# Kernel optimization log

Hardware: AMD Instinct MI355X
Metric: run time of the kernel (lower is better)

The kernel has to match this reference:

```python
import jax, jax.numpy as jnp
import numpy as np

N, E, DIM, NF, ED = 15000, 30000, 64, 3, 1

def _gru_cell(x, h, w_ih, w_hh, b_ih, b_hh):
    gi = x @ w_ih.T + b_ih
    gh = h @ w_hh.T + b_hh
    ir, iz, i_n = jnp.split(gi, 3, axis=-1)
    hr, hz, hn = jnp.split(gh, 3, axis=-1)
    r = jax.nn.sigmoid(ir + hr)
    z = jax.nn.sigmoid(iz + hz)
    n = jnp.tanh(i_n + r * hn)
    return (1.0 - z) * n + z * h

def _lstm_cell(x, h, c, w_ih, w_hh, b_ih, b_hh):
    g = x @ w_ih.T + b_ih + h @ w_hh.T + b_hh
    i, f, gg, o = jnp.split(g, 4, axis=-1)
    c2 = jax.nn.sigmoid(f) * c + jax.nn.sigmoid(i) * jnp.tanh(gg)
    return jax.nn.sigmoid(o) * jnp.tanh(c2), c2

def setup_inputs():
    key = jax.random.key(0)
    ks = jax.random.split(key, 32)
    p = lambda k, shape: jax.random.normal(k, shape, jnp.float32) * 0.05
    return {
        "x": jax.random.normal(ks[0], (N, NF), jnp.float32),
        "edge_index": jax.random.randint(ks[1], (2, E), 0, N),
        "edge_attr": jax.random.uniform(ks[2], (E, ED), jnp.float32),
        "lin0_w": p(ks[3], (DIM, NF)), "lin0_b": p(ks[4], (DIM,)),
        "e1_w": p(ks[5], (DIM, ED)), "e1_b": p(ks[6], (DIM,)),
        "e2_w": p(ks[7], (DIM * DIM, DIM)), "e2_b": p(ks[8], (DIM * DIM,)),
        "root_w": p(ks[9], (DIM, DIM)), "conv_b": p(ks[10], (DIM,)),
        "gru_w_ih": p(ks[11], (3 * DIM, DIM)), "gru_w_hh": p(ks[12], (3 * DIM, DIM)),
        "gru_b_ih": p(ks[13], (3 * DIM,)), "gru_b_hh": p(ks[14], (3 * DIM,)),
        "s2s_w_ih": p(ks[15], (4 * DIM, 2 * DIM)), "s2s_w_hh": p(ks[16], (4 * DIM, DIM)),
        "s2s_b_ih": p(ks[17], (4 * DIM,)), "s2s_b_hh": p(ks[18], (4 * DIM,)),
        "mem_w_ih": p(ks[19], (4 * DIM, 2 * DIM)), "mem_w_hh": p(ks[20], (4 * DIM, DIM)),
        "mem_b_ih": p(ks[21], (4 * DIM,)), "mem_b_hh": p(ks[22], (4 * DIM,)),
        "lin1_w": p(ks[23], (DIM, DIM)), "lin1_b": p(ks[24], (DIM,)),
        "lin3_w": p(ks[25], (1, DIM)), "lin3_b": p(ks[26], (1,)),
    }

def reference(x, edge_index, edge_attr, lin0_w, lin0_b, e1_w, e1_b, e2_w, e2_b,
              root_w, conv_b, gru_w_ih, gru_w_hh, gru_b_ih, gru_b_hh,
              s2s_w_ih, s2s_w_hh, s2s_b_ih, s2s_b_hh,
              mem_w_ih, mem_w_hh, mem_b_ih, mem_b_hh,
              lin1_w, lin1_b, lin3_w, lin3_b):
    n = x.shape[0]
    src, dst = edge_index[0], edge_index[1]
    # per-edge weight matrices from the edge MLP: [E, DIM, DIM] (edge_attr is constant across the 6 conv steps)
    he = jax.nn.relu(edge_attr @ e1_w.T + e1_b)
    We = (he @ e2_w.T + e2_b).reshape(-1, DIM, DIM)
    deg = jax.ops.segment_sum(jnp.ones(src.shape[0], jnp.float32), dst, num_segments=n)
    denom = jnp.maximum(deg, 1.0)[:, None]
    out = jax.nn.relu(x @ lin0_w.T + lin0_b)   # [N, DIM]
    h = out                                    # GRU hidden init = lin0 output
    for _ in range(6):
        msg = jnp.einsum('ei,eio->eo', out[src], We)          # gather + per-edge matmul
        agg = jax.ops.segment_sum(msg, dst, num_segments=n) / denom  # mean aggr
        m = jax.nn.relu(agg + out @ root_w + conv_b)          # NNConv root + bias
        h = _gru_cell(m, h, gru_w_ih, gru_w_hh, gru_b_ih, gru_b_hh)
        out = h
    # Set2Set pooling over a single graph (data.batch is all zeros)
    q_star = jnp.zeros((1, 2 * DIM), x.dtype)
    hs = jnp.zeros((1, DIM), x.dtype)
    cs = jnp.zeros((1, DIM), x.dtype)
    for _ in range(6):
        hs, cs = _lstm_cell(q_star, hs, cs, s2s_w_ih, s2s_w_hh, s2s_b_ih, s2s_b_hh)
        e = out @ hs[0]                     # [N] attention logits
        a = jax.nn.softmax(e)
        r = (a[:, None] * out).sum(0, keepdims=True)  # [1, DIM]
        q_star = jnp.concatenate([hs, r], axis=-1)     # [1, 2*DIM]
    hx, cx = _lstm_cell(q_star, jnp.zeros((1, DIM), x.dtype), jnp.zeros((1, DIM), x.dtype),
                        mem_w_ih, mem_w_hh, mem_b_ih, mem_b_hh)
    o = jax.nn.relu(hx @ lin1_w.T + lin1_b)
    v = o @ lin3_w.T + lin3_b               # [1, 1]
    return v, hx, cx
```

## Files before the change

### kernel.cpp

```cpp
#include <hip/hip_runtime.h>
#include <math.h>

#define Nn 15000
#define NP 15040
#define Ee 30000
#define NB_E 118
#define EB 938

#define OFF_AGG   0
#define OFF_DEG   962560
#define ZERO_END  977560
#define OFF_OUT   977568
#define OFF_DINV  1940128
#define OFF_AT    1955136
#define OFF_BT    2221376
#define OFF_BP    2487616
#define OFF_U     2487680
#define OFF_V     2491840
#define OFF_MC    2496000
#define OFF_PE    2496016
#define OFF_BH    2526016
#define OFF_BC    2533696
#define OFF_SS    2541376
#define OFF_SD    2571376
#define OFF_SA    2601376
#define OFF_SP    2631376
#define OFF_PK    2661376
#define OFF_GMA   2690048
#define OFF_GSA   2690304
#define OFF_GRA   2690560
#define OFF_GMB   2706944
#define OFF_GSB   2707200
#define OFF_GRB   2707456
#define OFF_HS    2723840
#define OFF_CS    2723904
#define OFF_TSA   2723968
#define OFF_TSB   2740352
#define OFF_TMA   2756736
#define OFF_TMB   2773120
#define WS_FLOATS 2789504

#define SB_LIN0   3760
#define SB_PAT    3760
#define SB_WT2    3761
#define SB_WT3    3873
#define SB_ZERO   4129
#define SB_TOTAL  5084
#define ZERO_F4   244390

__device__ __forceinline__ float sigf(float x) { return 1.0f / (1.0f + expf(-x)); }
__device__ __forceinline__ float bcast(float v, int l) {
    return __int_as_float(__builtin_amdgcn_readlane(__float_as_int(v), l));
}
__device__ __forceinline__ int bcasti(int v, int l) {
    return __builtin_amdgcn_readlane(v, l);
}

__global__ __launch_bounds__(256) void k_setup(
        const float* __restrict__ x, const float* __restrict__ l0w,
        const float* __restrict__ l0b, float* __restrict__ out,
        const float* __restrict__ e1w, const float* __restrict__ e1b,
        float* __restrict__ bp, float* __restrict__ u, float* __restrict__ v,
        int* __restrict__ mc,
        const float* __restrict__ rootw, const float* __restrict__ whh,
        const float* __restrict__ wih, float* __restrict__ pk,
        const float* __restrict__ swih, const float* __restrict__ swhh,
        const float* __restrict__ mwih,
        float* __restrict__ tsa, float* __restrict__ tsb,
        float* __restrict__ tma, float* __restrict__ tmb,
        float* __restrict__ zbase) {
    int b = blockIdx.x, tid = threadIdx.x;
    if (b < SB_LIN0) {
        int idx = b*256 + tid;
        int n = idx >> 6, o = idx & 63;
        float vv = 0.f;
        if (n < Nn)
            vv = fmaxf(l0b[o] + x[n*3+0]*l0w[o*3+0] + x[n*3+1]*l0w[o*3+1]
                       + x[n*3+2]*l0w[o*3+2], 0.f);
        out[idx] = vv;
    } else if (b == SB_PAT) {
        __shared__ float t[64]; __shared__ int valid[64];
        __shared__ float sbp[65]; __shared__ int cnt;
        int k = tid;
        float w1 = 0.f, b1 = 0.f, tv = 0.f; int va = 0;
        if (k < 64) {
            w1 = e1w[k]; b1 = e1b[k];
            if (w1 != 0.f) { tv = -b1 / w1; va = (tv > 0.f && tv < 1.f) ? 1 : 0; }
            t[k] = tv; valid[k] = va;
        }
        __syncthreads();
        if (k < 64 && va) {
            int rank = 0;
            for (int kk = 0; kk < 64; ++kk)
                if (valid[kk] && (t[kk] < tv || (t[kk] == tv && kk < k))) rank++;
            sbp[rank] = tv;
        }
        if (k == 0) { int c = 0; for (int kk = 0; kk < 64; ++kk) c += valid[kk]; cnt = c; *mc = c; }
        __syncthreads();
        if (k < 64) {
            int m = cnt;
            if (k < m) bp[k] = sbp[k];
            for (int j = 0; j <= m; ++j) {
                float lo = (j == 0) ? 0.f : sbp[j-1];
                float hi = (j == m) ? 1.f : sbp[j];
                float c = 0.5f * (lo + hi);
                int msk = (c * w1 + b1) > 0.f;
                u[j*64 + k] = msk ? w1 : 0.f;
                v[j*64 + k] = msk ? b1 : 0.f;
            }
        }
    } else if (b < SB_WT3) {
        int idx = (b - SB_WT2)*256 + tid;
        int g = idx >> 12;
        int t2 = idx & 4095;
        int q4 = t2 >> 2, k = t2 & 3;
        int lane = q4 & 63;
        int i4 = q4 >> 6;
        int i = i4*4 + k;
        float vv;
        if (g == 0)      vv = rootw[i*64 + lane];
        else if (g < 4)  vv = whh[((g-1)*64 + lane)*64 + i];
        else             vv = wih[((g-4)*64 + lane)*64 + i];
        pk[idx] = vv;
    } else if (b < SB_ZERO) {
        int idx = (b - SB_WT3)*256 + tid;
        int t2 = idx >> 14, r = idx & 16383;
        int i = r >> 8, g = r & 255;
        if (t2 == 0)      tsa[r] = swih[g*128 + i] + swhh[g*64 + i];
        else if (t2 == 1) tsb[r] = swih[g*128 + 64 + i];
        else if (t2 == 2) tma[r] = mwih[g*128 + i];
        else              tmb[r] = mwih[g*128 + 64 + i];
    } else {
        int idx = (b - SB_ZERO)*256 + tid;
        if (idx < ZERO_F4)
            ((float4*)zbase)[idx] = make_float4(0.f, 0.f, 0.f, 0.f);
    }
}

__global__ __launch_bounds__(256) void k_prep(
        const float* __restrict__ e2w, const float* __restrict__ e2b,
        const float* __restrict__ u, const float* __restrict__ v,
        const int* __restrict__ mc, float* __restrict__ At, float* __restrict__ Bt,
        const int* __restrict__ ei, const float* __restrict__ ea,
        const float* __restrict__ bp, float* __restrict__ deg,
        int* __restrict__ pe, int* __restrict__ bh) {
    int b = blockIdx.x, tid = threadIdx.x;
    if (b < 1040) {
        int j = b >> 4;
        if (j > *mc) return;
        int qc = b & 15;
        __shared__ float su[64], sv[64];
        if (tid < 64) { su[tid] = u[j*64+tid]; sv[tid] = v[j*64+tid]; }
        __syncthreads();
        int q = qc*256 + tid;
        int i = q >> 6, o = q & 63;
        const float* row = e2w + q*64;
        float a = 0.f, bb = 0.f;
        #pragma unroll 8
        for (int k = 0; k < 64; ++k) { float w = row[k]; a = fmaf(su[k], w, a); bb = fmaf(sv[k], w, bb); }
        At[j*4096 + o*64 + i] = a;
        Bt[j*4096 + o*64 + i] = bb + e2b[q];
    } else {
        int eb = b - 1040;
        __shared__ int lh[65];
        if (tid < 65) lh[tid] = 0;
        __syncthreads();
        int e = eb * 256 + tid;
        if (e < Ee) {
            atomicAdd(&deg[ei[Ee + e]], 1.0f);
            float a = ea[e];
            int m = *mc, p = 0;
            for (int j = 0; j < m; ++j) p += (bp[j] <= a) ? 1 : 0;
            pe[e] = p;
            atomicAdd(&lh[p], 1);
        }
        __syncthreads();
        if (tid < 65) bh[eb*65 + tid] = lh[tid];
    }
}

__global__ void k_scan2(const float* __restrict__ deg, float* __restrict__ dinv,
                        const int* __restrict__ bh, int* __restrict__ bc) {
    int tid = threadIdx.x;
    if (blockIdx.x < 59) {
        int n = blockIdx.x * 256 + tid;
        if (n < Nn) dinv[n] = 1.0f / fmaxf(deg[n], 1.0f);
        return;
    }
    __shared__ int stot[65]; __shared__ int sbase[65];
    if (tid < 65) {
        int t = 0;
        for (int b = 0; b < NB_E; ++b) t += bh[b*65 + tid];
        stot[tid] = t;
    }
    __syncthreads();
    if (tid == 0) {
        int run = 0;
        for (int j = 0; j < 65; ++j) { sbase[j] = run; run += stot[j]; }
    }
    __syncthreads();
    if (tid < 65) {
        int run = sbase[tid];
        for (int b = 0; b < NB_E; ++b) { bc[b*65 + tid] = run; run += bh[b*65 + tid]; }
    }
}

__global__ void k_scatter2(const int* __restrict__ ei, const float* __restrict__ ea,
                           const int* __restrict__ pe, const int* __restrict__ bc,
                           int* __restrict__ sS, int* __restrict__ sD,
                           float* __restrict__ sA, int* __restrict__ sP) {
    __shared__ int cur[65];
    int tid = threadIdx.x;
    if (tid < 65) cur[tid] = bc[blockIdx.x*65 + tid];
    __syncthreads();
    int e = blockIdx.x * 256 + tid;
    if (e >= Ee) return;
    int p = pe[e];
    int pos = atomicAdd(&cur[p], 1);
    sS[pos] = ei[e]; sD[pos] = ei[Ee + e]; sA[pos] = ea[e]; sP[pos] = p;
}

__global__ __launch_bounds__(256) void k_edge4(
        const int* __restrict__ sS, const int* __restrict__ sD,
        const float* __restrict__ sA, const int* __restrict__ sP,
        const float* __restrict__ out, const float* __restrict__ At,
        const float* __restrict__ Bt, const float* __restrict__ dinv,
        float* __restrict__ agg) {
    int tid = threadIdx.x, lane = tid & 63;
    int wid = (blockIdx.x * 256 + tid) >> 6;
    const int CH = 8;
    int e0 = wid * CH;
    if (e0 >= Ee) return;
    int e1 = e0 + CH; if (e1 > Ee) e1 = Ee;
    int cnt = e1 - e0;

    int eidx = e0 + lane;
    int msrc = 0, mdst = 0, mp = 0; float ma = 0.f, mdv = 0.f;
    if (lane < cnt) {
        msrc = sS[eidx]; mdst = sD[eidx]; ma = sA[eidx]; mp = sP[eidx];
        mdv = dinv[mdst];
    }

    float Ar[64], Br[64];
    int curp = -1;
    float hv_next = out[bcasti(msrc, 0)*64 + lane];
    for (int j = 0; j < cnt; ++j) {
        float hv = hv_next;
        if (j+1 < cnt) hv_next = out[bcasti(msrc, j+1)*64 + lane];
        int p = bcasti(mp, j);
        if (p != curp) {
            curp = p;
            const float4* Ap4 = (const float4*)(At + p*4096 + lane*64);
            const float4* Bp4 = (const float4*)(Bt + p*4096 + lane*64);
            #pragma unroll
            for (int q = 0; q < 16; ++q) {
                float4 av = Ap4[q], bv = Bp4[q];
                Ar[q*4+0]=av.x; Ar[q*4+1]=av.y; Ar[q*4+2]=av.z; Ar[q*4+3]=av.w;
                Br[q*4+0]=bv.x; Br[q*4+1]=bv.y; Br[q*4+2]=bv.z; Br[q*4+3]=bv.w;
            }
        }
        float a = bcast(ma, j);
        float acc0 = 0.f, acc1 = 0.f;
        #pragma unroll
        for (int i = 0; i < 64; i += 2) {
            float h0 = bcast(hv, i);
            float h1 = bcast(hv, i+1);
            acc0 = fmaf(h0, fmaf(a, Ar[i],   Br[i]),   acc0);
            acc1 = fmaf(h1, fmaf(a, Ar[i+1], Br[i+1]), acc1);
        }
        float acc = (acc0 + acc1) * bcast(mdv, j);
        atomicAdd(&agg[bcasti(mdst, j)*64 + lane], acc);
    }
}

__global__ __launch_bounds__(512, 2) void k_gru9(
        float* __restrict__ out, float* __restrict__ agg,
        const float* __restrict__ pk, const float* __restrict__ convb,
        const float* __restrict__ gbih, const float* __restrict__ gbhh) {
    __shared__ __align__(16) float wL[7*4096];
    int tid = threadIdx.x, lane = tid & 63, w = tid >> 6;
    {
        const float4* src = (const float4*)pk;
        float4* dst = (float4*)wL;
        #pragma unroll
        for (int i = 0; i < 14; ++i) dst[i*512 + tid] = src[i*512 + tid];
    }
    __syncthreads();
    const float4* wL4 = (const float4*)wL;
    int n0 = blockIdx.x*64 + w*8;

    float hv[8], mv[8], ghr[8], ghz[8], ghn[8];
    #pragma unroll
    for (int k = 0; k < 8; ++k) hv[k] = out[(n0+k)*64 + lane];

    float a0[8], a1[8], a2[8], a3[8];
    #pragma unroll
    for (int k = 0; k < 8; ++k) { a0[k]=0.f; a1[k]=0.f; a2[k]=0.f; a3[k]=0.f; }
    #pragma unroll 4
    for (int i4 = 0; i4 < 16; ++i4) {
        float4 w0 = wL4[(0*16+i4)*64 + lane];
        float4 w1 = wL4[(1*16+i4)*64 + lane];
        float4 w2 = wL4[(2*16+i4)*64 + lane];
        float4 w3 = wL4[(3*16+i4)*64 + lane];
        #pragma unroll
        for (int k = 0; k < 8; ++k) {
            float h;
            h = bcast(hv[k], i4*4+0);
            a0[k]=fmaf(h,w0.x,a0[k]); a1[k]=fmaf(h,w1.x,a1[k]);
            a2[k]=fmaf(h,w2.x,a2[k]); a3[k]=fmaf(h,w3.x,a3[k]);
            h = bcast(hv[k], i4*4+1);
            a0[k]=fmaf(h,w0.y,a0[k]); a1[k]=fmaf(h,w1.y,a1[k]);
            a2[k]=fmaf(h,w2.y,a2[k]); a3[k]=fmaf(h,w3.y,a3[k]);
            h = bcast(hv[k], i4*4+2);
            a0[k]=fmaf(h,w0.z,a0[k]); a1[k]=fmaf(h,w1.z,a1[k]);
            a2[k]=fmaf(h,w2.z,a2[k]); a3[k]=fmaf(h,w3.z,a3[k]);
            h = bcast(hv[k], i4*4+3);
            a0[k]=fmaf(h,w0.w,a0[k]); a1[k]=fmaf(h,w1.w,a1[k]);
            a2[k]=fmaf(h,w2.w,a2[k]); a3[k]=fmaf(h,w3.w,a3[k]);
        }
    }
    float cbv = convb[lane];
    #pragma unroll
    for (int k = 0; k < 8; ++k) {
        int gi = (n0+k)*64 + lane;
        float av = agg[gi]; agg[gi] = 0.f;
        mv[k] = fmaxf(a0[k] + av + cbv, 0.f);
        ghr[k] = a1[k]; ghz[k] = a2[k]; ghn[k] = a3[k];
    }

    #pragma unroll
    for (int k = 0; k < 8; ++k) { a0[k]=0.f; a1[k]=0.f; a2[k]=0.f; }
    #pragma unroll 4
    for (int i4 = 0; i4 < 16; ++i4) {
        float4 w4v = wL4[(4*16+i4)*64 + lane];
        float4 w5v = wL4[(5*16+i4)*64 + lane];
        float4 w6v = wL4[(6*16+i4)*64 + lane];
        #pragma unroll
        for (int k = 0; k < 8; ++k) {
            float h;
            h = bcast(mv[k], i4*4+0);
            a0[k]=fmaf(h,w4v.x,a0[k]); a1[k]=fmaf(h,w5v.x,a1[k]); a2[k]=fmaf(h,w6v.x,a2[k]);
            h = bcast(mv[k], i4*4+1);
            a0[k]=fmaf(h,w4v.y,a0[k]); a1[k]=fmaf(h,w5v.y,a1[k]); a2[k]=fmaf(h,w6v.y,a2[k]);
            h = bcast(mv[k], i4*4+2);
            a0[k]=fmaf(h,w4v.z,a0[k]); a1[k]=fmaf(h,w5v.z,a1[k]); a2[k]=fmaf(h,w6v.z,a2[k]);
            h = bcast(mv[k], i4*4+3);
            a0[k]=fmaf(h,w4v.w,a0[k]); a1[k]=fmaf(h,w5v.w,a1[k]); a2[k]=fmaf(h,w6v.w,a2[k]);
        }
    }

    float br  = gbih[lane]      + gbhh[lane];
    float bz  = gbih[64+lane]   + gbhh[64+lane];
    float bnI = gbih[128+lane];
    float bnH = gbhh[128+lane];
    #pragma unroll
    for (int k = 0; k < 8; ++k) {
        float r  = sigf(a0[k] + ghr[k] + br);
        float z  = sigf(a1[k] + ghz[k] + bz);
        float nn = tanhf(fmaf(r, ghn[k] + bnH, a2[k] + bnI));
        out[(n0+k)*64 + lane] = (1.f - z)*nn + z*hv[k];
    }
}

__global__ __launch_bounds__(512) void k_s2s(
        const float* __restrict__ tsa, const float* __restrict__ tsb,
        const float* __restrict__ bih, const float* __restrict__ bhh,
        float* __restrict__ hs, float* __restrict__ cs,
        const float* __restrict__ out,
        const float* __restrict__ gmax_rd, const float* __restrict__ gsum_rd,
        const float* __restrict__ gr_rd,
        float* __restrict__ gmax_wr, float* __restrict__ gsum_wr,
        float* __restrict__ gr_wr, int it) {
    __shared__ float red[512], shs[64], scs[64], srv[64], sg[256];
    __shared__ float wred[8], zred[8];
    __shared__ float sm_m[8], sm_z[8], sm_r[8][64];
    int tid = threadIdx.x, lane = tid & 63, w = tid >> 6;
    if (it == 0) {
        if (tid < 64) { shs[tid] = 0.f; scs[tid] = 0.f; srv[tid] = 0.f; }
        __syncthreads();
    } else {
        float gm = (tid < 256) ? gmax_rd[tid] : -3.4e38f;
        float wm = gm;
        #pragma unroll
        for (int off = 32; off > 0; off >>= 1) wm = fmaxf(wm, __shfl_xor(wm, off, 64));
        if (lane == 0) wred[w] = wm;
        __syncthreads();
        float M = fmaxf(fmaxf(fmaxf(wred[0], wred[1]), fmaxf(wred[2], wred[3])),
                        fmaxf(fmaxf(wred[4], wred[5]), fmaxf(wred[6], wred[7])));
        float zt = (tid < 256) ? gsum_rd[tid] * expf(gm - M) : 0.f;
        #pragma unroll
        for (int off = 32; off > 0; off >>= 1) zt += __shfl_xor(zt, off, 64);
        if (lane == 0) zred[w] = zt;
        float racc = 0.f;
        for (int b2 = w; b2 < 256; b2 += 8)
            racc = fmaf(gr_rd[b2*64 + lane], expf(gmax_rd[b2] - M), racc);
        red[tid] = racc;
        if (tid < 64) { shs[tid] = hs[tid]; scs[tid] = cs[tid]; }
        __syncthreads();
        if (w == 0) {
            float Z = zred[0]+zred[1]+zred[2]+zred[3]+zred[4]+zred[5]+zred[6]+zred[7];
            float s = 0.f;
            #pragma unroll
            for (int k = 0; k < 8; ++k) s += red[k*64 + lane];
            srv[lane] = s / Z;
        }
        __syncthreads();
    }
    if (tid < 256) {
        float g = bih[tid] + bhh[tid];
        #pragma unroll 8
        for (int i = 0; i < 64; ++i)
            g += shs[i]*tsa[i*256 + tid] + srv[i]*tsb[i*256 + tid];
        sg[tid] = g;
    }
    __syncthreads();
    if (tid < 64) {
        float ii = sigf(sg[tid]), ff = sigf(sg[64+tid]);
        float gg = tanhf(sg[128+tid]), oo = sigf(sg[192+tid]);
        float c2 = ff*scs[tid] + ii*gg;
        float hn = oo*tanhf(c2);
        shs[tid] = hn;
        if (blockIdx.x == 0) { hs[tid] = hn; cs[tid] = c2; }
    }
    __syncthreads();
    float hsv = shs[lane];
    float m = -3.4e38f, Z2 = 0.f, racc2 = 0.f;
    for (int n = blockIdx.x*8 + w; n < Nn; n += 2048) {
        float ov = out[n*64 + lane];
        float p = ov * hsv;
        #pragma unroll
        for (int off = 32; off > 0; off >>= 1) p += __shfl_xor(p, off, 64);
        float mn = fmaxf(m, p);
        float sc = expf(m - mn);
        float t  = expf(p - mn);
        Z2 = fmaf(Z2, sc, t);
        racc2 = fmaf(racc2, sc, t*ov);
        m = mn;
    }
    if (lane == 0) { sm_m[w] = m; sm_z[w] = Z2; }
    sm_r[w][lane] = racc2;
    __syncthreads();
    if (w == 0) {
        float M = sm_m[0];
        #pragma unroll
        for (int j = 1; j < 8; ++j) M = fmaxf(M, sm_m[j]);
        float Zb = 0.f, rb = 0.f;
        #pragma unroll
        for (int j = 0; j < 8; ++j) {
            float e = expf(sm_m[j] - M);
            Zb = fmaf(sm_z[j], e, Zb);
            rb = fmaf(sm_r[j][lane], e, rb);
        }
        gr_wr[blockIdx.x*64 + lane] = rb;
        if (lane == 0) { gmax_wr[blockIdx.x] = M; gsum_wr[blockIdx.x] = Zb; }
    }
}

__global__ __launch_bounds__(256) void k_final2(
        const float* __restrict__ tma, const float* __restrict__ tmb,
        const float* __restrict__ mbih, const float* __restrict__ mbhh,
        const float* __restrict__ hs,
        const float* __restrict__ gmax, const float* __restrict__ gsum,
        const float* __restrict__ gr,
        const float* __restrict__ l1w, const float* __restrict__ l1b,
        const float* __restrict__ l3w, const float* __restrict__ l3b,
        float* __restrict__ dout) {
    __shared__ float red[256], shs[64], srv[64], sg[256], shx[64], so[64];
    __shared__ float wred[4], zred[4];
    int tid = threadIdx.x, lane = tid & 63, w = tid >> 6;
    {
        float gm = gmax[tid];
        float wm = gm;
        #pragma unroll
        for (int off = 32; off > 0; off >>= 1) wm = fmaxf(wm, __shfl_xor(wm, off, 64));
        if (lane == 0) wred[w] = wm;
        __syncthreads();
        float M = fmaxf(fmaxf(wred[0], wred[1]), fmaxf(wred[2], wred[3]));
        float zt = gsum[tid] * expf(gm - M);
        #pragma unroll
        for (int off = 32; off > 0; off >>= 1) zt += __shfl_xor(zt, off, 64);
        if (lane == 0) zred[w] = zt;
        float racc = 0.f;
        for (int b2 = w; b2 < 256; b2 += 4)
            racc = fmaf(gr[b2*64 + lane], expf(gmax[b2] - M), racc);
        red[tid] = racc;
        if (tid < 64) shs[tid] = hs[tid];
        __syncthreads();
        if (w == 0) {
            float Z = zred[0]+zred[1]+zred[2]+zred[3];
            srv[lane] = (red[lane] + red[64+lane] + red[128+lane] + red[192+lane]) / Z;
        }
    }
    __syncthreads();
    {
        float g = mbih[tid] + mbhh[tid];
        #pragma unroll 8
        for (int i = 0; i < 64; ++i)
            g += shs[i]*tma[i*256 + tid] + srv[i]*tmb[i*256 + tid];
        sg[tid] = g;
    }
    __syncthreads();
    if (tid < 64) {
        float ii = sigf(sg[tid]);
        float gg = tanhf(sg[128+tid]);
        float oo = sigf(sg[192+tid]);
        float c2 = ii * gg;
        float hx = oo * tanhf(c2);
        shx[tid] = hx;
        dout[1 + tid] = hx;
        dout[65 + tid] = c2;
    }
    __syncthreads();
    if (tid < 64) {
        float a = l1b[tid];
        const float* wr = l1w + tid*64;
        #pragma unroll 8
        for (int i = 0; i < 64; ++i) a = fmaf(shx[i], wr[i], a);
        so[tid] = fmaxf(a, 0.f);
    }
    __syncthreads();
    if (tid == 0) {
        float v = l3b[0];
        for (int i = 0; i < 64; ++i) v = fmaf(so[i], l3w[i], v);
        dout[0] = v;
    }
}

extern "C" void kernel_launch(void* const* d_in, const int* in_sizes, int n_in,
                              void* d_out, int out_size, void* d_ws, size_t ws_size,
                              hipStream_t stream) {
    const float* x    = (const float*)d_in[0];
    const int*   ei   = (const int*)  d_in[1];
    const float* ea   = (const float*)d_in[2];
    const float* l0w  = (const float*)d_in[3];
    const float* l0b  = (const float*)d_in[4];
    const float* e1w  = (const float*)d_in[5];
    const float* e1b  = (const float*)d_in[6];
    const float* e2w  = (const float*)d_in[7];
    const float* e2b  = (const float*)d_in[8];
    const float* rootw= (const float*)d_in[9];
    const float* convb= (const float*)d_in[10];
    const float* gwih = (const float*)d_in[11];
    const float* gwhh = (const float*)d_in[12];
    const float* gbih = (const float*)d_in[13];
    const float* gbhh = (const float*)d_in[14];
    const float* swih = (const float*)d_in[15];
    const float* swhh = (const float*)d_in[16];
    const float* sbih = (const float*)d_in[17];
    const float* sbhh = (const float*)d_in[18];
    const float* mwih = (const float*)d_in[19];
    const float* mbih = (const float*)d_in[21];
    const float* mbhh = (const float*)d_in[22];
    const float* l1w  = (const float*)d_in[23];
    const float* l1b  = (const float*)d_in[24];
    const float* l3w  = (const float*)d_in[25];
    const float* l3b  = (const float*)d_in[26];

    float* ws   = (float*)d_ws;
    float* dout = (float*)d_out;
    if (ws_size < (size_t)WS_FLOATS * sizeof(float)) return;

    float* agg  = ws + OFF_AGG;
    float* deg  = ws + OFF_DEG;
    float* out  = ws + OFF_OUT;
    float* dinv = ws + OFF_DINV;
    float* At   = ws + OFF_AT;
    float* Bt   = ws + OFF_BT;
    float* bp   = ws + OFF_BP;
    float* ubuf = ws + OFF_U;
    float* vbuf = ws + OFF_V;
    int*   mc   = (int*)(ws + OFF_MC);
    int*   pe   = (int*)(ws + OFF_PE);
    int*   bh   = (int*)(ws + OFF_BH);
    int*   bc   = (int*)(ws + OFF_BC);
    int*   sS   = (int*)(ws + OFF_SS);
    int*   sD   = (int*)(ws + OFF_SD);
    float* sA   = ws + OFF_SA;
    int*   sP   = (int*)(ws + OFF_SP);
    float* pk   = ws + OFF_PK;
    float* gmA  = ws + OFF_GMA;
    float* gsA  = ws + OFF_GSA;
    float* grA  = ws + OFF_GRA;
    float* gmB  = ws + OFF_GMB;
    float* gsB  = ws + OFF_GSB;
    float* grB  = ws + OFF_GRB;
    float* hs   = ws + OFF_HS;
    float* cs   = ws + OFF_CS;
    float* tsa  = ws + OFF_TSA;
    float* tsb  = ws + OFF_TSB;
    float* tma  = ws + OFF_TMA;
    float* tmb  = ws + OFF_TMB;

    k_setup   <<<SB_TOTAL, 256, 0, stream>>>(x, l0w, l0b, out, e1w, e1b, bp, ubuf,
                                             vbuf, mc, rootw, gwhh, gwih, pk,
                                             swih, swhh, mwih, tsa, tsb, tma, tmb,
                                             ws + OFF_AGG);
    k_prep    <<<1040 + NB_E, 256, 0, stream>>>(e2w, e2b, ubuf, vbuf, mc, At, Bt,
                                                ei, ea, bp, deg, pe, bh);
    k_scan2   <<<60, 256, 0, stream>>>(deg, dinv, bh, bc);
    k_scatter2<<<NB_E, 256, 0, stream>>>(ei, ea, pe, bc, sS, sD, sA, sP);

    for (int s = 0; s < 6; ++s) {
        k_edge4<<<EB, 256, 0, stream>>>(sS, sD, sA, sP, out, At, Bt, dinv, agg);
        k_gru9 <<<NP/64, 512, 0, stream>>>(out, agg, pk, convb, gbih, gbhh);
    }

    for (int it = 0; it < 6; ++it) {
        float* gm_rd = (it & 1) ? gmA : gmB;
        float* gs_rd = (it & 1) ? gsA : gsB;
        float* gr_rd = (it & 1) ? grA : grB;
        float* gm_wr = (it & 1) ? gmB : gmA;
        float* gs_wr = (it & 1) ? gsB : gsA;
        float* gr_wr = (it & 1) ? grB : grA;
        k_s2s<<<256, 512, 0, stream>>>(tsa, tsb, sbih, sbhh, hs, cs, out,
                                       gm_rd, gs_rd, gr_rd, gm_wr, gs_wr, gr_wr, it);
    }

    k_final2<<<1, 256, 0, stream>>>(tma, tmb, mbih, mbhh, hs, gmB, gsB, grB,
                                    l1w, l1b, l3w, l3b, dout);
}
```

Baseline: 436.2 us.

## Fuse setup, prep, scan and scatter kernels; prefetch GRU inputs; double-buffer s2s state

The four setup launches (setup, prep, scan, scatter) become two. Every block that needs the edge-weight breakpoints now recomputes them in shared memory instead of reading them from a separate pass. The scatter kernel computes its own per-block prefix offsets from the histogram, so the separate scan pass goes away. The GRU kernel issues its loads of the node state and aggregation before staging the weights into shared memory, to overlap that latency, and the Set2Set hidden and cell state are ping-ponged between two buffers. The trade-offs are redundant per-block breakpoint and prefix work, and a dependence on the zeroing blocks running before the degree atomics in the same grid.

After: 439.3 us. No clear change (+0.7%).

```diff
diff --git a/kernel.cpp b/kernel.cpp
--- a/kernel.cpp
+++ b/kernel.cpp
@@ -14,13 +14,8 @@
 #define OFF_DINV  1940128
 #define OFF_AT    1955136
 #define OFF_BT    2221376
-#define OFF_BP    2487616
-#define OFF_U     2487680
-#define OFF_V     2491840
-#define OFF_MC    2496000
 #define OFF_PE    2496016
 #define OFF_BH    2526016
-#define OFF_BC    2533696
 #define OFF_SS    2541376
 #define OFF_SD    2571376
 #define OFF_SA    2601376
@@ -32,21 +27,23 @@
 #define OFF_GMB   2706944
 #define OFF_GSB   2707200
 #define OFF_GRB   2707456
-#define OFF_HS    2723840
-#define OFF_CS    2723904
 #define OFF_TSA   2723968
 #define OFF_TSB   2740352
 #define OFF_TMA   2756736
 #define OFF_TMB   2773120
-#define WS_FLOATS 2789504
-
-#define SB_LIN0   3760
-#define SB_PAT    3760
-#define SB_WT2    3761
-#define SB_WT3    3873
-#define SB_ZERO   4129
-#define SB_TOTAL  5084
-#define ZERO_F4   244390
+#define OFF_HSA   2789504
+#define OFF_CSA   2789568
+#define OFF_HSB   2789632
+#define OFF_CSB   2789696
+#define WS_FLOATS 2789760
+
+#define SA_L0_END   3760
+#define SA_WT2_END  3872
+#define SA_WT3_END  4128
+#define SA_Z_END    5083
+#define SA_AB_END   6123
+#define SA_EP_END   6241
+#define ZERO_F4     244390
 
 __device__ __forceinline__ float sigf(float x) { return 1.0f / (1.0f + expf(-x)); }
 __device__ __forceinline__ float bcast(float v, int l) {
@@ -56,21 +53,23 @@
     return __builtin_amdgcn_readlane(v, l);
 }
 
-__global__ __launch_bounds__(256) void k_setup(
+__global__ __launch_bounds__(256) void k_setupAll(
         const float* __restrict__ x, const float* __restrict__ l0w,
         const float* __restrict__ l0b, float* __restrict__ out,
         const float* __restrict__ e1w, const float* __restrict__ e1b,
-        float* __restrict__ bp, float* __restrict__ u, float* __restrict__ v,
-        int* __restrict__ mc,
+        const float* __restrict__ e2w, const float* __restrict__ e2b,
+        float* __restrict__ At, float* __restrict__ Bt,
         const float* __restrict__ rootw, const float* __restrict__ whh,
         const float* __restrict__ wih, float* __restrict__ pk,
         const float* __restrict__ swih, const float* __restrict__ swhh,
         const float* __restrict__ mwih,
         float* __restrict__ tsa, float* __restrict__ tsb,
         float* __restrict__ tma, float* __restrict__ tmb,
-        float* __restrict__ zbase) {
+        float* __restrict__ zbase,
+        const int* __restrict__ ei, const float* __restrict__ ea,
+        float* __restrict__ deg, int* __restrict__ pe, int* __restrict__ bh) {
     int b = blockIdx.x, tid = threadIdx.x;
-    if (b < SB_LIN0) {
+    if (b < SA_L0_END) {
         int idx = b*256 + tid;
         int n = idx >> 6, o = idx & 63;
         float vv = 0.f;
@@ -78,39 +77,8 @@
             vv = fmaxf(l0b[o] + x[n*3+0]*l0w[o*3+0] + x[n*3+1]*l0w[o*3+1]
                        + x[n*3+2]*l0w[o*3+2], 0.f);
         out[idx] = vv;
-    } else if (b == SB_PAT) {
-        __shared__ float t[64]; __shared__ int valid[64];
-        __shared__ float sbp[65]; __shared__ int cnt;
-        int k = tid;
-        float w1 = 0.f, b1 = 0.f, tv = 0.f; int va = 0;
-        if (k < 64) {
-            w1 = e1w[k]; b1 = e1b[k];
-            if (w1 != 0.f) { tv = -b1 / w1; va = (tv > 0.f && tv < 1.f) ? 1 : 0; }
-            t[k] = tv; valid[k] = va;
-        }
-        __syncthreads();
-        if (k < 64 && va) {
-            int rank = 0;
-            for (int kk = 0; kk < 64; ++kk)
-                if (valid[kk] && (t[kk] < tv || (t[kk] == tv && kk < k))) rank++;
-            sbp[rank] = tv;
-        }
-        if (k == 0) { int c = 0; for (int kk = 0; kk < 64; ++kk) c += valid[kk]; cnt = c; *mc = c; }
-        __syncthreads();
-        if (k < 64) {
-            int m = cnt;
-            if (k < m) bp[k] = sbp[k];
-            for (int j = 0; j <= m; ++j) {
-                float lo = (j == 0) ? 0.f : sbp[j-1];
-                float hi = (j == m) ? 1.f : sbp[j];
-                float c = 0.5f * (lo + hi);
-                int msk = (c * w1 + b1) > 0.f;
-                u[j*64 + k] = msk ? w1 : 0.f;
-                v[j*64 + k] = msk ? b1 : 0.f;
-            }
-        }
-    } else if (b < SB_WT3) {
-        int idx = (b - SB_WT2)*256 + tid;
+    } else if (b < SA_WT2_END) {
+        int idx = (b - SA_L0_END)*256 + tid;
         int g = idx >> 12;
         int t2 = idx & 4095;
         int q4 = t2 >> 2, k = t2 & 3;
@@ -122,35 +90,49 @@
         else if (g < 4)  vv = whh[((g-1)*64 + lane)*64 + i];
         else             vv = wih[((g-4)*64 + lane)*64 + i];
         pk[idx] = vv;
-    } else if (b < SB_ZERO) {
-        int idx = (b - SB_WT3)*256 + tid;
+    } else if (b < SA_WT3_END) {
+        int idx = (b - SA_WT2_END)*256 + tid;
         int t2 = idx >> 14, r = idx & 16383;
         int i = r >> 8, g = r & 255;
         if (t2 == 0)      tsa[r] = swih[g*128 + i] + swhh[g*64 + i];
         else if (t2 == 1) tsb[r] = swih[g*128 + 64 + i];
         else if (t2 == 2) tma[r] = mwih[g*128 + i];
         else              tmb[r] = mwih[g*128 + 64 + i];
-    } else {
-        int idx = (b - SB_ZERO)*256 + tid;
+    } else if (b < SA_Z_END) {
+        int idx = (b - SA_WT3_END)*256 + tid;
         if (idx < ZERO_F4)
             ((float4*)zbase)[idx] = make_float4(0.f, 0.f, 0.f, 0.f);
-    }
-}
-
-__global__ __launch_bounds__(256) void k_prep(
-        const float* __restrict__ e2w, const float* __restrict__ e2b,
-        const float* __restrict__ u, const float* __restrict__ v,
-        const int* __restrict__ mc, float* __restrict__ At, float* __restrict__ Bt,
-        const int* __restrict__ ei, const float* __restrict__ ea,
-        const float* __restrict__ bp, float* __restrict__ deg,
-        int* __restrict__ pe, int* __restrict__ bh) {
-    int b = blockIdx.x, tid = threadIdx.x;
-    if (b < 1040) {
-        int j = b >> 4;
-        if (j > *mc) return;
-        int qc = b & 15;
+    } else if (b < SA_AB_END) {
+        __shared__ float t[64]; __shared__ int valid[64];
+        __shared__ float sbp[65]; __shared__ int cnt;
         __shared__ float su[64], sv[64];
-        if (tid < 64) { su[tid] = u[j*64+tid]; sv[tid] = v[j*64+tid]; }
+        int rel = b - SA_Z_END;
+        int j = rel >> 4, qc = rel & 15;
+        float w1 = 0.f, b1 = 0.f, tv = 0.f; int va = 0;
+        if (tid < 64) {
+            w1 = e1w[tid]; b1 = e1b[tid];
+            if (w1 != 0.f) { tv = -b1 / w1; va = (tv > 0.f && tv < 1.f) ? 1 : 0; }
+            t[tid] = tv; valid[tid] = va;
+        }
+        __syncthreads();
+        if (tid < 64 && va) {
+            int rank = 0;
+            for (int kk = 0; kk < 64; ++kk)
+                if (valid[kk] && (t[kk] < tv || (t[kk] == tv && kk < tid))) rank++;
+            sbp[rank] = tv;
+        }
+        if (tid == 0) { int c = 0; for (int kk = 0; kk < 64; ++kk) c += valid[kk]; cnt = c; }
+        __syncthreads();
+        int m = cnt;
+        if (j > m) return;
+        if (tid < 64) {
+            float lo = (j == 0) ? 0.f : sbp[j-1];
+            float hi = (j == m) ? 1.f : sbp[j];
+            float c = 0.5f * (lo + hi);
+            int msk = (c * w1 + b1) > 0.f;
+            su[tid] = msk ? w1 : 0.f;
+            sv[tid] = msk ? b1 : 0.f;
+        }
         __syncthreads();
         int q = qc*256 + tid;
         int i = q >> 6, o = q & 63;
@@ -161,16 +143,33 @@
         At[j*4096 + o*64 + i] = a;
         Bt[j*4096 + o*64 + i] = bb + e2b[q];
     } else {
-        int eb = b - 1040;
+        __shared__ float t[64]; __shared__ int valid[64];
+        __shared__ float sbp[65]; __shared__ int cnt;
         __shared__ int lh[65];
+        int eb = b - SA_AB_END;
+        float w1 = 0.f, b1 = 0.f, tv = 0.f; int va = 0;
+        if (tid < 64) {
+            w1 = e1w[tid]; b1 = e1b[tid];
+            if (w1 != 0.f) { tv = -b1 / w1; va = (tv > 0.f && tv < 1.f) ? 1 : 0; }
+            t[tid] = tv; valid[tid] = va;
+        }
         if (tid < 65) lh[tid] = 0;
         __syncthreads();
+        if (tid < 64 && va) {
+            int rank = 0;
+            for (int kk = 0; kk < 64; ++kk)
+                if (valid[kk] && (t[kk] < tv || (t[kk] == tv && kk < tid))) rank++;
+            sbp[rank] = tv;
+        }
+        if (tid == 0) { int c = 0; for (int kk = 0; kk < 64; ++kk) c += valid[kk]; cnt = c; }
+        __syncthreads();
+        int m = cnt;
         int e = eb * 256 + tid;
         if (e < Ee) {
             atomicAdd(&deg[ei[Ee + e]], 1.0f);
             float a = ea[e];
-            int m = *mc, p = 0;
-            for (int j = 0; j < m; ++j) p += (bp[j] <= a) ? 1 : 0;
+            int p = 0;
+            for (int jj = 0; jj < m; ++jj) p += (sbp[jj] <= a) ? 1 : 0;
             pe[e] = p;
             atomicAdd(&lh[p], 1);
         }
@@ -179,19 +178,28 @@
     }
 }
 
-__global__ void k_scan2(const float* __restrict__ deg, float* __restrict__ dinv,
-                        const int* __restrict__ bh, int* __restrict__ bc) {
+__global__ __launch_bounds__(256) void k_scatter3(
+        const float* __restrict__ deg, float* __restrict__ dinv,
+        const int* __restrict__ ei, const float* __restrict__ ea,
+        const int* __restrict__ pe, const int* __restrict__ bh,
+        int* __restrict__ sS, int* __restrict__ sD,
+        float* __restrict__ sA, int* __restrict__ sP) {
     int tid = threadIdx.x;
     if (blockIdx.x < 59) {
         int n = blockIdx.x * 256 + tid;
         if (n < Nn) dinv[n] = 1.0f / fmaxf(deg[n], 1.0f);
         return;
     }
-    __shared__ int stot[65]; __shared__ int sbase[65];
+    int eb = blockIdx.x - 59;
+    __shared__ int stot[65], sown[65], sbase[65], cur[65];
     if (tid < 65) {
-        int t = 0;
-        for (int b = 0; b < NB_E; ++b) t += bh[b*65 + tid];
-        stot[tid] = t;
+        int own = 0, tot = 0;
+        for (int b2 = 0; b2 < NB_E; ++b2) {
+            int v = bh[b2*65 + tid];
+            if (b2 < eb) own += v;
+            tot += v;
+        }
+        stot[tid] = tot; sown[tid] = own;
     }
     __syncthreads();
     if (tid == 0) {
@@ -199,21 +207,9 @@
         for (int j = 0; j < 65; ++j) { sbase[j] = run; run += stot[j]; }
     }
     __syncthreads();
-    if (tid < 65) {
-        int run = sbase[tid];
-        for (int b = 0; b < NB_E; ++b) { bc[b*65 + tid] = run; run += bh[b*65 + tid]; }
-    }
-}
-
-__global__ void k_scatter2(const int* __restrict__ ei, const float* __restrict__ ea,
-                           const int* __restrict__ pe, const int* __restrict__ bc,
-                           int* __restrict__ sS, int* __restrict__ sD,
-                           float* __restrict__ sA, int* __restrict__ sP) {
-    __shared__ int cur[65];
-    int tid = threadIdx.x;
-    if (tid < 65) cur[tid] = bc[blockIdx.x*65 + tid];
-    __syncthreads();
-    int e = blockIdx.x * 256 + tid;
+    if (tid < 65) cur[tid] = sbase[tid] + sown[tid];
+    __syncthreads();
+    int e = eb * 256 + tid;
     if (e >= Ee) return;
     int p = pe[e];
     int pos = atomicAdd(&cur[p], 1);
@@ -279,6 +275,18 @@
         const float* __restrict__ gbih, const float* __restrict__ gbhh) {
     __shared__ __align__(16) float wL[7*4096];
     int tid = threadIdx.x, lane = tid & 63, w = tid >> 6;
+    int n0 = blockIdx.x*64 + w*8;
+
+    float hv[8], av[8];
+    #pragma unroll
+    for (int k = 0; k < 8; ++k) hv[k] = out[(n0+k)*64 + lane];
+    #pragma unroll
+    for (int k = 0; k < 8; ++k) {
+        int gi = (n0+k)*64 + lane;
+        av[k] = agg[gi];
+        agg[gi] = 0.f;
+    }
+
     {
         const float4* src = (const float4*)pk;
         float4* dst = (float4*)wL;
@@ -287,12 +295,8 @@
     }
     __syncthreads();
     const float4* wL4 = (const float4*)wL;
-    int n0 = blockIdx.x*64 + w*8;
-
-    float hv[8], mv[8], ghr[8], ghz[8], ghn[8];
-    #pragma unroll
-    for (int k = 0; k < 8; ++k) hv[k] = out[(n0+k)*64 + lane];
-
+
+    float mv[8], ghr[8], ghz[8], ghn[8];
     float a0[8], a1[8], a2[8], a3[8];
     #pragma unroll
     for (int k = 0; k < 8; ++k) { a0[k]=0.f; a1[k]=0.f; a2[k]=0.f; a3[k]=0.f; }
@@ -322,9 +326,7 @@
     float cbv = convb[lane];
     #pragma unroll
     for (int k = 0; k < 8; ++k) {
-        int gi = (n0+k)*64 + lane;
-        float av = agg[gi]; agg[gi] = 0.f;
-        mv[k] = fmaxf(a0[k] + av + cbv, 0.f);
+        mv[k] = fmaxf(a0[k] + av[k] + cbv, 0.f);
         ghr[k] = a1[k]; ghz[k] = a2[k]; ghn[k] = a3[k];
     }
 
@@ -365,7 +367,8 @@
 __global__ __launch_bounds__(512) void k_s2s(
         const float* __restrict__ tsa, const float* __restrict__ tsb,
         const float* __restrict__ bih, const float* __restrict__ bhh,
-        float* __restrict__ hs, float* __restrict__ cs,
+        const float* __restrict__ hs_rd, const float* __restrict__ cs_rd,
+        float* __restrict__ hs_wr, float* __restrict__ cs_wr,
         const float* __restrict__ out,
         const float* __restrict__ gmax_rd, const float* __restrict__ gsum_rd,
         const float* __restrict__ gr_rd,
@@ -395,7 +398,7 @@
         for (int b2 = w; b2 < 256; b2 += 8)
             racc = fmaf(gr_rd[b2*64 + lane], expf(gmax_rd[b2] - M), racc);
         red[tid] = racc;
-        if (tid < 64) { shs[tid] = hs[tid]; scs[tid] = cs[tid]; }
+        if (tid < 64) { shs[tid] = hs_rd[tid]; scs[tid] = cs_rd[tid]; }
         __syncthreads();
         if (w == 0) {
             float Z = zred[0]+zred[1]+zred[2]+zred[3]+zred[4]+zred[5]+zred[6]+zred[7];
@@ -420,7 +423,7 @@
         float c2 = ff*scs[tid] + ii*gg;
         float hn = oo*tanhf(c2);
         shs[tid] = hn;
-        if (blockIdx.x == 0) { hs[tid] = hn; cs[tid] = c2; }
+        if (blockIdx.x == 0) { hs_wr[tid] = hn; cs_wr[tid] = c2; }
     }
     __syncthreads();
     float hsv = shs[lane];
@@ -566,13 +569,8 @@
     float* dinv = ws + OFF_DINV;
     float* At   = ws + OFF_AT;
     float* Bt   = ws + OFF_BT;
-    float* bp   = ws + OFF_BP;
-    float* ubuf = ws + OFF_U;
-    float* vbuf = ws + OFF_V;
-    int*   mc   = (int*)(ws + OFF_MC);
     int*   pe   = (int*)(ws + OFF_PE);
     int*   bh   = (int*)(ws + OFF_BH);
-    int*   bc   = (int*)(ws + OFF_BC);
     int*   sS   = (int*)(ws + OFF_SS);
     int*   sD   = (int*)(ws + OFF_SD);
     float* sA   = ws + OFF_SA;
@@ -584,21 +582,21 @@
     float* gmB  = ws + OFF_GMB;
     float* gsB  = ws + OFF_GSB;
     float* grB  = ws + OFF_GRB;
-    float* hs   = ws + OFF_HS;
-    float* cs   = ws + OFF_CS;
     float* tsa  = ws + OFF_TSA;
     float* tsb  = ws + OFF_TSB;
     float* tma  = ws + OFF_TMA;
     float* tmb  = ws + OFF_TMB;
-
-    k_setup   <<<SB_TOTAL, 256, 0, stream>>>(x, l0w, l0b, out, e1w, e1b, bp, ubuf,
-                                             vbuf, mc, rootw, gwhh, gwih, pk,
-                                             swih, swhh, mwih, tsa, tsb, tma, tmb,
-                                             ws + OFF_AGG);
-    k_prep    <<<1040 + NB_E, 256, 0, stream>>>(e2w, e2b, ubuf, vbuf, mc, At, Bt,
-                                                ei, ea, bp, deg, pe, bh);
-    k_scan2   <<<60, 256, 0, stream>>>(deg, dinv, bh, bc);
-    k_scatter2<<<NB_E, 256, 0, stream>>>(ei, ea, pe, bc, sS, sD, sA, sP);
+    float* hsA  = ws + OFF_HSA;
+    float* csA  = ws + OFF_CSA;
+    float* hsB  = ws + OFF_HSB;
+    float* csB  = ws + OFF_CSB;
+
+    k_setupAll<<<SA_EP_END, 256, 0, stream>>>(x, l0w, l0b, out, e1w, e1b, e2w, e2b,
+                                              At, Bt, rootw, gwhh, gwih, pk,
+                                              swih, swhh, mwih, tsa, tsb, tma, tmb,
+                                              ws + OFF_AGG, ei, ea, deg, pe, bh);
+    k_scatter3<<<59 + NB_E, 256, 0, stream>>>(deg, dinv, ei, ea, pe, bh,
+                                              sS, sD, sA, sP);
 
     for (int s = 0; s < 6; ++s) {
         k_edge4<<<EB, 256, 0, stream>>>(sS, sD, sA, sP, out, At, Bt, dinv, agg);
@@ -609,13 +607,18 @@
         float* gm_rd = (it & 1) ? gmA : gmB;
         float* gs_rd = (it & 1) ? gsA : gsB;
         float* gr_rd = (it & 1) ? grA : grB;
+        float* hs_rd = (it & 1) ? hsA : hsB;
+        float* cs_rd = (it & 1) ? csA : csB;
         float* gm_wr = (it & 1) ? gmB : gmA;
         float* gs_wr = (it & 1) ? gsB : gsA;
         float* gr_wr = (it & 1) ? grB : grA;
-        k_s2s<<<256, 512, 0, stream>>>(tsa, tsb, sbih, sbhh, hs, cs, out,
+        float* hs_wr = (it & 1) ? hsB : hsA;
+        float* cs_wr = (it & 1) ? csB : csA;
+        k_s2s<<<256, 512, 0, stream>>>(tsa, tsb, sbih, sbhh, hs_rd, cs_rd,
+                                       hs_wr, cs_wr, out,
                                        gm_rd, gs_rd, gr_rd, gm_wr, gs_wr, gr_wr, it);
     }
 
-    k_final2<<<1, 256, 0, stream>>>(tma, tmb, mbih, mbhh, hs, gmB, gsB, grB,
+    k_final2<<<1, 256, 0, stream>>>(tma, tmb, mbih, mbhh, hsB, gmB, gsB, grB,
                                     l1w, l1b, l3w, l3b, dout);
 }
```
